# Optimization experiments

Hardware: AMD Instinct MI355X
Metric: run time of the kernel (lower is better)

The kernel has to match this reference:

```python
import jax, jax.numpy as jnp
import numpy as np

L, D, H, FF, I, MAXREL = 6, 512, 8, 2048, 50, 128
HD = D // H
NREL = 2 * MAXREL + 1
EPS = 1e-5


def setup_inputs() -> dict:
    key = jax.random.key(0)
    ks = jax.random.split(key, 32)
    s = 0.02
    p = {
        'x': jax.random.normal(ks[0], (16, 512, I), dtype=jnp.float32),
        'in_w': jax.random.normal(ks[1], (I, D)) * s,
        'in_b': jnp.zeros((D,), jnp.float32),
        'Wq': jax.random.normal(ks[2], (L, D, D)) * s,
        'Wk': jax.random.normal(ks[3], (L, D, D)) * s,
        'Wv': jax.random.normal(ks[4], (L, D, D)) * s,
        'Wo': jax.random.normal(ks[5], (L, D, D)) * s,
        'bo': jnp.zeros((L, D), jnp.float32),
        'rel_emb': jax.random.normal(ks[6], (L, NREL, HD)) * s,
        'w1': jax.random.normal(ks[7], (L, D, FF)) * s,
        'b1': jnp.zeros((L, FF), jnp.float32),
        'w2': jax.random.normal(ks[8], (L, FF, D)) * s,
        'b2': jnp.zeros((L, D), jnp.float32),
        'ln1_g': jnp.ones((L, D), jnp.float32),
        'ln1_b': jnp.zeros((L, D), jnp.float32),
        'ln2_g': jnp.ones((L, D), jnp.float32),
        'ln2_b': jnp.zeros((L, D), jnp.float32),
        'on_g': jnp.ones((D,), jnp.float32),
        'on_b': jnp.zeros((D,), jnp.float32),
        'p1_w': jax.random.normal(ks[9], (D, D // 2)) * s,
        'p1_b': jnp.zeros((D // 2,), jnp.float32),
        'p2_w': jax.random.normal(ks[10], (D // 2, 1)) * s,
        'p2_b': jnp.zeros((1,), jnp.float32),
    }
    return p


def _layer_norm(x, g, b):
    m = jnp.mean(x, axis=-1, keepdims=True)
    v = jnp.mean(jnp.square(x - m), axis=-1, keepdims=True)
    return (x - m) * jax.lax.rsqrt(v + EPS) * g + b


def _sinusoidal_pe(seq_len, d_model):
    pos = jnp.arange(seq_len, dtype=jnp.float32)[:, None]
    div = jnp.exp(jnp.arange(0, d_model, 2, dtype=jnp.float32) * (-jnp.log(10000.0) / d_model))
    pe = jnp.zeros((seq_len, d_model), jnp.float32)
    pe = pe.at[:, 0::2].set(jnp.sin(pos * div))
    pe = pe.at[:, 1::2].set(jnp.cos(pos * div))
    return pe


def reference(x, in_w, in_b, Wq, Wk, Wv, Wo, bo, rel_emb, w1, b1, w2, b2,
              ln1_g, ln1_b, ln2_g, ln2_b, on_g, on_b, p1_w, p1_b, p2_w, p2_b):
    B, S, _ = x.shape
    scale = jnp.sqrt(jnp.float32(HD))
    # relative position index matrix [S, S] in [0, 2*MAXREL]
    r = jnp.arange(S)
    rel_idx = jnp.clip(r[None, :] - r[:, None], -MAXREL, MAXREL) + MAXREL

    h = x @ in_w + in_b                       # [B,S,D]
    h = h + _sinusoidal_pe(S, D)

    for l in range(L):
        q = (h @ Wq[l]).reshape(B, S, H, HD).transpose(0, 2, 1, 3)  # [B,H,S,hd]
        k = (h @ Wk[l]).reshape(B, S, H, HD).transpose(0, 2, 1, 3)
        v = (h @ Wv[l]).reshape(B, S, H, HD).transpose(0, 2, 1, 3)
        scores = jnp.einsum('bhqd,bhkd->bhqk', q, k) / scale
        rel = rel_emb[l][rel_idx]             # [S,S,hd]
        scores = scores + jnp.einsum('bhqd,qkd->bhqk', q, rel)  # rel bias is NOT scaled (matches source)
        attn = jax.nn.softmax(scores, axis=-1)
        ctx = jnp.einsum('bhqk,bhkd->bhqd', attn, v)
        ctx = ctx.transpose(0, 2, 1, 3).reshape(B, S, D)
        attn_out = ctx @ Wo[l] + bo[l]
        h = _layer_norm(h + attn_out, ln1_g[l], ln1_b[l])
        ff = jax.nn.relu(h @ w1[l] + b1[l]) @ w2[l] + b2[l]
        h = _layer_norm(h + ff, ln2_g[l], ln2_b[l])

    h = _layer_norm(h, on_g, on_b)
    out = jax.nn.relu(h @ p1_w + p1_b) @ p2_w + p2_b  # [B,S,1]
    return out
```

## Files before the change

kernel.cpp:

```cpp
#include <hip/hip_runtime.h>

typedef unsigned short u16;
typedef unsigned int   u32;
typedef short   short8  __attribute__((ext_vector_type(8)));
typedef float   floatx4 __attribute__((ext_vector_type(4)));
typedef int     intx4   __attribute__((ext_vector_type(4)));

#define NTOK 8192
#define SEQ  512
#define NLAYER 6

#define OFF_WT   ((size_t)0)
#define OFF_HB   ((size_t)38010880)
#define OFF_QKV  ((size_t)46399488)
#define OFF_CTX  ((size_t)71565312)
#define OFF_GOUT ((size_t)79953920)
#define OFF_FF   ((size_t)96731136)
#define OFF_HD1  ((size_t)130285568)
#define OFF_VT   OFF_FF
#define OFF_RELB OFF_HD1

#define LSTRIDE 3145728
#define P1T_OFF 18874368

__device__ __forceinline__ float b2f(u16 v) { return __uint_as_float(((u32)v) << 16); }
__device__ __forceinline__ float lo16(u32 v) { return __uint_as_float(v << 16); }
__device__ __forceinline__ float hi16(u32 v) { return __uint_as_float(v & 0xffff0000u); }
__device__ __forceinline__ u16 f2b(float f) {
  u32 x = __float_as_uint(f);
  return (u16)((x + 0x7fffu + ((x >> 16) & 1u)) >> 16);
}
__device__ __forceinline__ u32 pack2(float a, float b) {
  return (u32)f2b(a) | ((u32)f2b(b) << 16);
}
__device__ __forceinline__ u32 cvtpk(float a, float b) {
  u32 r;
  asm("v_cvt_pk_bf16_f32 %0, %1, %2" : "=v"(r) : "v"(a), "v"(b));
  return r;
}

typedef __attribute__((address_space(1))) void* gas_t;
typedef __attribute__((address_space(3))) void* las_t;

__global__ __launch_bounds__(256) void transpose_all(
    const float* __restrict__ Wq, const float* __restrict__ Wk,
    const float* __restrict__ Wv, const float* __restrict__ Wo,
    const float* __restrict__ w1, const float* __restrict__ w2,
    const float* __restrict__ p1, u16* __restrict__ wT)
{
  __shared__ u16 tile[64][65];
  const int tb = blockIdx.x;
  const float* src; u16* dst; int R, C, tidx;
  if (tb < 4608) {
    const int l = tb / 768, r = tb % 768;
    const size_t lofs = (size_t)l * LSTRIDE;
    if (r < 256) {
      const int m = r >> 6; tidx = r & 63; R = 512; C = 512;
      const float* bases[4] = {Wq, Wk, Wv, Wo};
      src = bases[m] + (size_t)l * 262144;
      dst = wT + lofs + (size_t)m * 262144;
    } else if (r < 512) {
      tidx = r - 256; R = 512; C = 2048;
      src = w1 + (size_t)l * 1048576; dst = wT + lofs + 1048576;
    } else {
      tidx = r - 512; R = 2048; C = 512;
      src = w2 + (size_t)l * 1048576; dst = wT + lofs + 2097152;
    }
  } else {
    tidx = tb - 4608; R = 512; C = 256;
    src = p1; dst = wT + P1T_OFF;
  }
  const int tcn = C >> 6;
  const int tr = tidx / tcn, tc = tidx % tcn;
  const int th = threadIdx.x;
  {
    const int lr = th >> 2, cg = (th & 3) * 16;
    const float* sp = src + (size_t)(tr*64 + lr) * C + tc*64 + cg;
    float4 f0 = *(const float4*)(sp);
    float4 f1 = *(const float4*)(sp + 4);
    float4 f2 = *(const float4*)(sp + 8);
    float4 f3 = *(const float4*)(sp + 12);
    u16* tp = &tile[lr][cg];
    tp[0]=f2b(f0.x); tp[1]=f2b(f0.y); tp[2]=f2b(f0.z); tp[3]=f2b(f0.w);
    tp[4]=f2b(f1.x); tp[5]=f2b(f1.y); tp[6]=f2b(f1.z); tp[7]=f2b(f1.w);
    tp[8]=f2b(f2.x); tp[9]=f2b(f2.y); tp[10]=f2b(f2.z); tp[11]=f2b(f2.w);
    tp[12]=f2b(f3.x); tp[13]=f2b(f3.y); tp[14]=f2b(f3.z); tp[15]=f2b(f3.w);
  }
  __syncthreads();
  {
    const int oc = th >> 2, rg = (th & 3) * 16;
    u32 wds[8];
    #pragma unroll
    for (int i = 0; i < 8; ++i)
      wds[i] = (u32)tile[rg + 2*i][oc] | ((u32)tile[rg + 2*i + 1][oc] << 16);
    const int n  = tc*64 + oc;
    const int k0 = tr*64 + rg;
    const int nb = n >> 7, j = (n >> 4) & 7, lr = n & 15;
    const int kc = k0 >> 5, lq = (k0 >> 3) & 3;
    const int KC = R >> 5;
    u16* base = dst + (((((size_t)nb*KC + kc) << 3) + j) << 9);
    uint4 o0; o0.x=wds[0]; o0.y=wds[1]; o0.z=wds[2]; o0.w=wds[3];
    uint4 o1; o1.x=wds[4]; o1.y=wds[5]; o1.z=wds[6]; o1.w=wds[7];
    *(uint4*)(base + (lq*16 + lr)*8)       = o0;
    *(uint4*)(base + ((lq+1)*16 + lr)*8)   = o1;
  }
}

__global__ __launch_bounds__(128) void input_proj(
    const float* __restrict__ x, const float* __restrict__ w, const float* __restrict__ ib,
    u16* __restrict__ hb)
{
  const int row = blockIdx.x, t = threadIdx.x;
  const int s = row & (SEQ - 1);
  __shared__ float xs[50];
  if (t < 50) xs[t] = x[row*50 + t];
  __syncthreads();
  const int d0 = t * 4;
  float4 acc = *(const float4*)(ib + d0);
  #pragma unroll
  for (int i = 0; i < 50; ++i) {
    const float4 wv = *(const float4*)(w + i*512 + d0);
    const float xv = xs[i];
    acc.x = fmaf(xv, wv.x, acc.x);
    acc.y = fmaf(xv, wv.y, acc.y);
    acc.z = fmaf(xv, wv.z, acc.z);
    acc.w = fmaf(xv, wv.w, acc.w);
  }
  const float cexp = -0.017988946f;
  const float dv0 = __expf((float)d0 * cexp);
  const float dv1 = __expf((float)(d0 + 2) * cexp);
  float s0, c0, s1, c1;
  __sincosf((float)s * dv0, &s0, &c0);
  __sincosf((float)s * dv1, &s1, &c1);
  acc.x += s0; acc.y += c0; acc.z += s1; acc.w += c1;
  u32* hp = (u32*)(hb + (size_t)row*512 + d0);
  hp[0] = pack2(acc.x, acc.y);
  hp[1] = pack2(acc.z, acc.w);
}

__global__ __launch_bounds__(256, 4) void gemm_bt(
    const u16* __restrict__ A, const u16* __restrict__ Bt,
    const float* __restrict__ bias,
    u16* __restrict__ outP0, u16* __restrict__ outP1, u16* __restrict__ outB,
    u16* __restrict__ vTout,
    const int M, const int N, const int K, const int kLen, const int flags)
{
  __shared__ __align__(16) u16 As[2][8192];
  const int id = blockIdx.x;
  const int xcd = id & 7, rest = id >> 3;
  const int bm = (rest & 7) * 8 + xcd;
  const int bn = rest >> 3;
  const int z = blockIdx.y;
  const int kOff = z * kLen;
  const int m0 = bm << 7, n0 = bn << 7;
  const int tid = threadIdx.x;
  const int wave = tid >> 6, lane = tid & 63;
  const int wr = (wave >> 1) << 6, wc = (wave & 1) << 6;
  const int lrow = lane & 15, lquad = lane >> 4;

  floatx4 acc[4][4];
  #pragma unroll
  for (int i = 0; i < 4; ++i)
    #pragma unroll
    for (int j = 0; j < 4; ++j) { floatx4 zz = {0.f,0.f,0.f,0.f}; acc[i][j] = zz; }

  const u16* a0p = A + (size_t)m0 * K + kOff;
  const int c0 = tid, c1 = 256 + tid;
  const int ar0 = c0 >> 2, as0 = (c0 & 3) * 8;
  const int ar1 = c1 >> 2, as1 = (c1 & 3) * 8;
  const int KC = K >> 5;
  const u16* bW = Bt + ((((size_t)bn*KC + (kOff >> 5)) * 8 + (wave & 1) * 4) << 9) + lane*8;

#define STAGE_A(buf, k0) do {                                                                  \
    __builtin_amdgcn_global_load_lds((gas_t)(a0p + (size_t)ar0*K + (k0) + as0),                \
                                     (las_t)(&As[buf][c0*8]), 16, 0, 0);                       \
    __builtin_amdgcn_global_load_lds((gas_t)(a0p + (size_t)ar1*K + (k0) + as1),                \
                                     (las_t)(&As[buf][c1*8]), 16, 0, 0);                       \
    __builtin_amdgcn_global_load_lds((gas_t)(a0p + (size_t)ar0*K + (k0) + 32 + as0),           \
                                     (las_t)(&As[buf][4096 + c0*8]), 16, 0, 0);                \
    __builtin_amdgcn_global_load_lds((gas_t)(a0p + (size_t)ar1*K + (k0) + 32 + as1),           \
                                     (las_t)(&As[buf][4096 + c1*8]), 16, 0, 0);                \
  } while (0)

  const int nst = kLen >> 6;
  STAGE_A(0, 0);
  __syncthreads();

  int cur = 0;
  for (int t = 0; t < nst; ++t) {
    const u16* bc = bW + (size_t)(2*t) * 4096;
    short8 b0[4], b1[4];
    #pragma unroll
    for (int j = 0; j < 4; ++j) b0[j] = *(const short8*)(bc + j*512);
    if (t + 1 < nst) STAGE_A(cur ^ 1, (t + 1) * 64);
    #pragma unroll
    for (int j = 0; j < 4; ++j) b1[j] = *(const short8*)(bc + 4096 + j*512);
    {
      short8 af[4];
      #pragma unroll
      for (int i = 0; i < 4; ++i) af[i] = *(const short8*)&As[cur][(wr + i*16 + lrow)*32 + lquad*8];
      #pragma unroll
      for (int i = 0; i < 4; ++i)
        #pragma unroll
        for (int j = 0; j < 4; ++j)
          acc[i][j] = __builtin_amdgcn_mfma_f32_16x16x32_bf16(b0[j], af[i], acc[i][j], 0, 0, 0);
    }
    {
      short8 af[4];
      #pragma unroll
      for (int i = 0; i < 4; ++i) af[i] = *(const short8*)&As[cur][4096 + (wr + i*16 + lrow)*32 + lquad*8];
      #pragma unroll
      for (int i = 0; i < 4; ++i)
        #pragma unroll
        for (int j = 0; j < 4; ++j)
          acc[i][j] = __builtin_amdgcn_mfma_f32_16x16x32_bf16(b1[j], af[i], acc[i][j], 0, 0, 0);
    }
    if (t + 1 < nst) { __syncthreads(); cur ^= 1; }
  }
#undef STAGE_A

  if ((flags & 4) && n0 >= 1024) {
    #pragma unroll
    for (int i = 0; i < 4; ++i) {
      const int row = m0 + wr + i*16 + lrow;
      const int bb = row >> 9, s = row & 511;
      #pragma unroll
      for (int j = 0; j < 4; ++j) {
        const int cm0 = (n0 - 1024) + wc + j*16 + lquad*4;
        #pragma unroll
        for (int v = 0; v < 4; ++v) {
          const int cm = cm0 + v;
          const int hh = cm >> 6, d = cm & 63;
          vTout[((size_t)(bb*8 + hh)*64 + d)*512 + s] = f2b(acc[i][j][v]);
        }
      }
    }
    return;
  }

  u16* outT = outB ? outB : ((z == 0) ? outP0 : outP1);
  const bool hasb = ((flags & 1) != 0) && (z == 0);
  const bool dorelu = (flags & 2) != 0;
  #pragma unroll
  for (int i = 0; i < 4; ++i) {
    const int row = m0 + wr + i*16 + lrow;
    #pragma unroll
    for (int j = 0; j < 4; ++j) {
      const int colbase = n0 + wc + j*16 + lquad*4;
      float4 bv4 = make_float4(0.f, 0.f, 0.f, 0.f);
      if (hasb) bv4 = *(const float4*)(bias + colbase);
      float v0 = acc[i][j][0] + bv4.x;
      float v1 = acc[i][j][1] + bv4.y;
      float v2 = acc[i][j][2] + bv4.z;
      float v3 = acc[i][j][3] + bv4.w;
      if (dorelu) {
        v0 = fmaxf(v0, 0.f); v1 = fmaxf(v1, 0.f);
        v2 = fmaxf(v2, 0.f); v3 = fmaxf(v3, 0.f);
      }
      const size_t off = (size_t)row * N + colbase;
      uint2 o; o.x = pack2(v0, v1); o.y = pack2(v2, v3);
      *(uint2*)(outT + off) = o;
    }
  }
}

__global__ __launch_bounds__(256) void cvt_rel_all(
    const float* __restrict__ rel, u16* __restrict__ relB)
{
  const int i = blockIdx.x*256 + threadIdx.x;
  if (i < 6*257*64) {
    const int l = i / 16448, rem = i % 16448;
    relB[l*17408 + rem] = f2b(rel[i]);
  }
}

__global__ __launch_bounds__(256, 3) void attn_mfma(
    const u16* __restrict__ qkv, const u16* __restrict__ vT,
    const u16* __restrict__ relB, u16* __restrict__ ctx)
{
  const int id = blockIdx.x;
  const int xcd = id & 7, g = (id >> 3) & 15, qt = id >> 7;
  const int bh = xcd*16 + g;
  const int b = bh >> 3, h = bh & 7;
  const int t = threadIdx.x, w = t >> 6, lane = t & 63;
  const int lr = lane & 15, quad = lane >> 4;

  __shared__ __align__(16) u16 Ks[64*72];
  __shared__ __align__(16) u16 Vs[64*72];
  __shared__ __align__(16) u16 Pr[64*274];

  const size_t token0 = (size_t)b*512 + qt*64;
  const int srow = t >> 2, scol = (t & 3) * 16;
  const u16* kbase = qkv + (size_t)b*512*1536 + 512 + h*64;
  const u16* vbase = vT + (size_t)bh*64*512;

  short8 af0, af1;
  {
    const u16* qp = qkv + (token0 + w*16 + lr)*1536 + h*64 + quad*8;
    af0 = *(const short8*)(qp);
    af1 = *(const short8*)(qp + 32);
  }

  uint4 kr0, kr1, vr0, vr1;
  {
    const u16* kp = kbase + (size_t)srow*1536 + scol;
    kr0 = *(const uint4*)kp; kr1 = *(const uint4*)(kp + 8);
    const u16* vp = vbase + (size_t)srow*512 + scol;
    vr0 = *(const uint4*)vp; vr1 = *(const uint4*)(vp + 8);
  }

  #pragma unroll 4
  for (int nt = 0; nt < 17; ++nt) {
    const u16* rp = relB + (nt*16 + lr)*64 + quad*8;
    short8 rb0 = *(const short8*)(rp);
    short8 rb1 = *(const short8*)(rp + 32);
    floatx4 c = {0.f,0.f,0.f,0.f};
    c = __builtin_amdgcn_mfma_f32_16x16x32_bf16(af0, rb0, c, 0, 0, 0);
    c = __builtin_amdgcn_mfma_f32_16x16x32_bf16(af1, rb1, c, 0, 0, 0);
    #pragma unroll
    for (int r = 0; r < 4; ++r)
      Pr[(w*16 + quad*4 + r)*274 + nt*16 + lr] = f2b(c[r] * 1.44269504f);
  }

  floatx4 oacc[4];
  float lacc = 0.f;
  #pragma unroll
  for (int n = 0; n < 4; ++n) { floatx4 zz = {0.f,0.f,0.f,0.f}; oacc[n] = zz; }

  const int qglob = qt*64 + w*16 + lr;
  const int prbase = (w*16 + lr)*274 + 128;

  const float prLo = b2f(Pr[prbase - 128]);
  const float prHi = b2f(Pr[prbase + 128]);

  for (int kt = 0; kt < 8; ++kt) {
    __syncthreads();
    *(uint4*)&Ks[srow*72 + scol]     = kr0;
    *(uint4*)&Ks[srow*72 + scol + 8] = kr1;
    *(uint4*)&Vs[srow*72 + scol]     = vr0;
    *(uint4*)&Vs[srow*72 + scol + 8] = vr1;
    __syncthreads();

    if (kt < 7) {
      const u16* kp = kbase + (size_t)((kt+1)*64 + srow)*1536 + scol;
      kr0 = *(const uint4*)kp; kr1 = *(const uint4*)(kp + 8);
      const u16* vp = vbase + (size_t)srow*512 + (kt+1)*64 + scol;
      vr0 = *(const uint4*)vp; vr1 = *(const uint4*)(vp + 8);
    }

    floatx4 s4[4];
    __builtin_amdgcn_s_setprio(1);
    #pragma unroll
    for (int nt = 0; nt < 4; ++nt) {
      short8 kb0 = *(const short8*)&Ks[(nt*16 + lr)*72 + quad*8];
      short8 kb1 = *(const short8*)&Ks[(nt*16 + lr)*72 + 32 + quad*8];
      floatx4 c = {0.f,0.f,0.f,0.f};
      c = __builtin_amdgcn_mfma_f32_16x16x32_bf16(kb0, af0, c, 0, 0, 0);
      c = __builtin_amdgcn_mfma_f32_16x16x32_bf16(kb1, af1, c, 0, 0, 0);
      s4[nt] = c;
    }
    __builtin_amdgcn_s_setprio(0);

    const int tmin = kt*64 - (qt*64 + w*16 + 15);
    const int tmax = tmin + 78;
    u32 wq[4][2];
    const int kq = kt*64 + quad*4 - qglob;
    if (tmin >= 128 || tmax <= -128) {
      const float pc = (tmin >= 128) ? prHi : prLo;
      #pragma unroll
      for (int nt = 0; nt < 4; ++nt) {
        float p[4];
        #pragma unroll
        for (int r = 0; r < 4; ++r)
          p[r] = exp2f(fmaf(s4[nt][r], 0.18033688f, pc));
        lacc += (p[0] + p[1]) + (p[2] + p[3]);
        wq[nt][0] = cvtpk(p[0], p[1]);
        wq[nt][1] = cvtpk(p[2], p[3]);
      }
    } else if (tmin >= -128 && tmax <= 128) {
      #pragma unroll
      for (int nt = 0; nt < 4; ++nt) {
        const int dbase = kq + nt*16;
        float p[4];
        #pragma unroll
        for (int r = 0; r < 4; ++r)
          p[r] = exp2f(fmaf(s4[nt][r], 0.18033688f, b2f(Pr[prbase + dbase + r])));
        lacc += (p[0] + p[1]) + (p[2] + p[3]);
        wq[nt][0] = cvtpk(p[0], p[1]);
        wq[nt][1] = cvtpk(p[2], p[3]);
      }
    } else {
      #pragma unroll
      for (int nt = 0; nt < 4; ++nt) {
        const int dbase = kq + nt*16;
        float p[4];
        #pragma unroll
        for (int r = 0; r < 4; ++r) {
          int dd = dbase + r;
          dd = dd < -128 ? -128 : (dd > 128 ? 128 : dd);
          p[r] = exp2f(fmaf(s4[nt][r], 0.18033688f, b2f(Pr[prbase + dd])));
        }
        lacc += (p[0] + p[1]) + (p[2] + p[3]);
        wq[nt][0] = cvtpk(p[0], p[1]);
        wq[nt][1] = cvtpk(p[2], p[3]);
      }
    }

    intx4 pw0; pw0.x = (int)wq[0][0]; pw0.y = (int)wq[0][1];
               pw0.z = (int)wq[1][0]; pw0.w = (int)wq[1][1];
    intx4 pw1; pw1.x = (int)wq[2][0]; pw1.y = (int)wq[2][1];
               pw1.z = (int)wq[3][0]; pw1.w = (int)wq[3][1];
    const short8 pf0 = __builtin_bit_cast(short8, pw0);
    const short8 pf1 = __builtin_bit_cast(short8, pw1);

    __builtin_amdgcn_s_setprio(1);
    #pragma unroll
    for (int nd = 0; nd < 4; ++nd) {
      const int vrow = (nd*16 + lr)*72;
      uint2 a0 = *(const uint2*)&Vs[vrow + quad*4];
      uint2 a1 = *(const uint2*)&Vs[vrow + 16 + quad*4];
      uint2 a2 = *(const uint2*)&Vs[vrow + 32 + quad*4];
      uint2 a3 = *(const uint2*)&Vs[vrow + 48 + quad*4];
      intx4 v0; v0.x = (int)a0.x; v0.y = (int)a0.y; v0.z = (int)a1.x; v0.w = (int)a1.y;
      intx4 v1; v1.x = (int)a2.x; v1.y = (int)a2.y; v1.z = (int)a3.x; v1.w = (int)a3.y;
      const short8 vb0 = __builtin_bit_cast(short8, v0);
      const short8 vb1 = __builtin_bit_cast(short8, v1);
      oacc[nd] = __builtin_amdgcn_mfma_f32_16x16x32_bf16(vb0, pf0, oacc[nd], 0, 0, 0);
      oacc[nd] = __builtin_amdgcn_mfma_f32_16x16x32_bf16(vb1, pf1, oacc[nd], 0, 0, 0);
    }
    __builtin_amdgcn_s_setprio(0);
  }

  lacc += __shfl_xor(lacc, 16);
  lacc += __shfl_xor(lacc, 32);

  {
    const float inv = 1.f / lacc;
    u16* cp = ctx + (token0 + w*16 + lr)*512 + h*64;
    #pragma unroll
    for (int nd = 0; nd < 4; ++nd) {
      const int d = nd*16 + quad*4;
      uint2 o;
      o.x = pack2(oacc[nd][0]*inv, oacc[nd][1]*inv);
      o.y = pack2(oacc[nd][2]*inv, oacc[nd][3]*inv);
      *(uint2*)(cp + d) = o;
    }
  }
}

__global__ __launch_bounds__(256) void ln_kernel(
    const u16* __restrict__ resB, const u16* __restrict__ add0,
    const u16* __restrict__ add1,
    const float* __restrict__ g, const float* __restrict__ be,
    u16* __restrict__ hb)
{
  const int wv = threadIdx.x >> 6, ln = threadIdx.x & 63;
  const int row = blockIdx.x * 4 + wv;
  const size_t base = (size_t)row * 512;
  const int off = ln * 8;

  const uint4 rv = *(const uint4*)(resB + base + off);
  float x[8];
  x[0] = lo16(rv.x); x[1] = hi16(rv.x);
  x[2] = lo16(rv.y); x[3] = hi16(rv.y);
  x[4] = lo16(rv.z); x[5] = hi16(rv.z);
  x[6] = lo16(rv.w); x[7] = hi16(rv.w);
  if (add0) {
    const uint4 a = *(const uint4*)(add0 + base + off);
    x[0] += lo16(a.x); x[1] += hi16(a.x);
    x[2] += lo16(a.y); x[3] += hi16(a.y);
    x[4] += lo16(a.z); x[5] += hi16(a.z);
    x[6] += lo16(a.w); x[7] += hi16(a.w);
  }
  if (add1) {
    const uint4 a = *(const uint4*)(add1 + base + off);
    x[0] += lo16(a.x); x[1] += hi16(a.x);
    x[2] += lo16(a.y); x[3] += hi16(a.y);
    x[4] += lo16(a.z); x[5] += hi16(a.z);
    x[6] += lo16(a.w); x[7] += hi16(a.w);
  }

  float s = ((x[0]+x[1]) + (x[2]+x[3])) + ((x[4]+x[5]) + (x[6]+x[7]));
  #pragma unroll
  for (int o = 1; o < 64; o <<= 1) s += __shfl_xor(s, o);
  const float mean = s * (1.f/512.f);

  float vs = 0.f;
  #pragma unroll
  for (int i = 0; i < 8; ++i) { const float d = x[i] - mean; vs = fmaf(d, d, vs); }
  #pragma unroll
  for (int o = 1; o < 64; o <<= 1) vs += __shfl_xor(vs, o);
  const float inv = 1.f / sqrtf(vs * (1.f/512.f) + 1e-5f);

  const float4 g0 = *(const float4*)(g + off);
  const float4 g1 = *(const float4*)(g + off + 4);
  const float4 b0 = *(const float4*)(be + off);
  const float4 b1 = *(const float4*)(be + off + 4);
  const float y0 = (x[0]-mean)*inv*g0.x + b0.x;
  const float y1 = (x[1]-mean)*inv*g0.y + b0.y;
  const float y2 = (x[2]-mean)*inv*g0.z + b0.z;
  const float y3 = (x[3]-mean)*inv*g0.w + b0.w;
  const float y4 = (x[4]-mean)*inv*g1.x + b1.x;
  const float y5 = (x[5]-mean)*inv*g1.y + b1.y;
  const float y6 = (x[6]-mean)*inv*g1.z + b1.z;
  const float y7 = (x[7]-mean)*inv*g1.w + b1.w;
  uint4 o;
  o.x = pack2(y0, y1); o.y = pack2(y2, y3);
  o.z = pack2(y4, y5); o.w = pack2(y6, y7);
  *(uint4*)(hb + base + off) = o;
}

__global__ __launch_bounds__(256) void head2_kernel(
    const u16* __restrict__ hd1, const float* __restrict__ p2w,
    const float* __restrict__ p2b, float* __restrict__ out)
{
  const int wv = threadIdx.x >> 6, ln = threadIdx.x & 63;
  const int row = blockIdx.x * 4 + wv;
  const u16* hp = hd1 + (size_t)row * 256 + ln*4;
  const u32 h0 = *(const u32*)hp, h1 = *(const u32*)(hp + 2);
  const float4 w = *(const float4*)(p2w + ln*4);
  float acc = lo16(h0)*w.x + hi16(h0)*w.y + lo16(h1)*w.z + hi16(h1)*w.w;
  #pragma unroll
  for (int off = 1; off < 64; off <<= 1) acc += __shfl_xor(acc, off);
  if (ln == 0) out[row] = acc + p2b[0];
}

extern "C" void kernel_launch(void* const* d_in, const int* in_sizes, int n_in,
                              void* d_out, int out_size, void* d_ws, size_t ws_size,
                              hipStream_t stream) {
  (void)in_sizes; (void)n_in; (void)out_size; (void)ws_size;
  const float* X    = (const float*)d_in[0];
  const float* INW  = (const float*)d_in[1];
  const float* INB  = (const float*)d_in[2];
  const float* WQ   = (const float*)d_in[3];
  const float* WK   = (const float*)d_in[4];
  const float* WV   = (const float*)d_in[5];
  const float* WO   = (const float*)d_in[6];
  const float* BO   = (const float*)d_in[7];
  const float* REL  = (const float*)d_in[8];
  const float* W1   = (const float*)d_in[9];
  const float* B1   = (const float*)d_in[10];
  const float* W2   = (const float*)d_in[11];
  const float* B2   = (const float*)d_in[12];
  const float* LN1G = (const float*)d_in[13];
  const float* LN1B = (const float*)d_in[14];
  const float* LN2G = (const float*)d_in[15];
  const float* LN2B = (const float*)d_in[16];
  const float* ONG  = (const float*)d_in[17];
  const float* ONB  = (const float*)d_in[18];
  const float* P1W  = (const float*)d_in[19];
  const float* P1B  = (const float*)d_in[20];
  const float* P2W  = (const float*)d_in[21];
  const float* P2B  = (const float*)d_in[22];
  float* out = (float*)d_out;

  char* ws = (char*)d_ws;
  u16*   wT    = (u16*)(ws + OFF_WT);
  u16*   hB    = (u16*)(ws + OFF_HB);
  u16*   qkv   = (u16*)(ws + OFF_QKV);
  u16*   ctx   = (u16*)(ws + OFF_CTX);
  u16*   gout0 = (u16*)(ws + OFF_GOUT);
  u16*   gout1 = (u16*)(ws + OFF_QKV);
  u16*   ff    = (u16*)(ws + OFF_FF);
  u16*   hd1   = (u16*)(ws + OFF_HD1);
  u16*   vTb   = (u16*)(ws + OFF_VT);
  u16*   relBa = (u16*)(ws + OFF_RELB);

  transpose_all<<<4640, 256, 0, stream>>>(WQ, WK, WV, WO, W1, W2, P1W, wT);
  cvt_rel_all<<<386, 256, 0, stream>>>(REL, relBa);
  input_proj<<<NTOK, 128, 0, stream>>>(X, INW, INB, hB);

  for (int l = 0; l < NLAYER; ++l) {
    const u16* wTl = wT + (size_t)l * LSTRIDE;
    gemm_bt<<<dim3(768,1), 256, 0, stream>>>(hB, wTl, nullptr, nullptr, nullptr, qkv, vTb,
                                             8192, 1536, 512, 512, 4);
    attn_mfma<<<1024, 256, 0, stream>>>(qkv, vTb, relBa + l*17408, ctx);
    gemm_bt<<<dim3(256,2), 256, 0, stream>>>(ctx, wTl + 786432, BO + l*512,
                                             gout0, gout1, nullptr, nullptr,
                                             8192, 512, 512, 256, 1);
    ln_kernel<<<2048, 256, 0, stream>>>(hB, gout0, gout1, LN1G + l*512, LN1B + l*512, hB);
    gemm_bt<<<dim3(1024,1), 256, 0, stream>>>(hB, wTl + 1048576, B1 + l*2048,
                                              nullptr, nullptr, ff, nullptr,
                                              8192, 2048, 512, 512, 3);
    gemm_bt<<<dim3(256,2), 256, 0, stream>>>(ff, wTl + 2097152, B2 + l*512,
                                             gout0, gout1, nullptr, nullptr,
                                             8192, 512, 2048, 1024, 1);
    ln_kernel<<<2048, 256, 0, stream>>>(hB, gout0, gout1, LN2G + l*512, LN2B + l*512, hB);
  }
  ln_kernel<<<2048, 256, 0, stream>>>(hB, nullptr, nullptr, ONG, ONB, hB);
  gemm_bt<<<dim3(128,1), 256, 0, stream>>>(hB, wT + P1T_OFF, P1B,
                                           nullptr, nullptr, hd1, nullptr,
                                           8192, 256, 512, 512, 3);
  head2_kernel<<<2048, 256, 0, stream>>>(hd1, P2W, P2B, out);
}
```

Baseline: 1.075 ms.

## Store activations in MFMA-packed layout and load GEMM A operand directly

Activations (hidden state, attention context, FF intermediate) are now written by producer kernels in the same fragment-packed layout already used for the transposed weights. This lets the GEMM load A fragments straight from global memory into registers, like B, and drop the LDS staging buffer and its barriers. The GEMM main loop is rewritten as a register double buffer, and the occupancy hint drops from 4 to 3 blocks to make room for the extra registers. The cost is scattered packed-index stores in the producers and more global traffic per wave, since nothing is shared through LDS.

```diff
diff --git a/kernel.cpp b/kernel.cpp
--- a/kernel.cpp
+++ b/kernel.cpp
@@ -11,10 +11,10 @@
 #define NLAYER 6
 
 #define OFF_WT   ((size_t)0)
-#define OFF_HB   ((size_t)38010880)
 #define OFF_QKV  ((size_t)46399488)
 #define OFF_CTX  ((size_t)71565312)
 #define OFF_GOUT ((size_t)79953920)
+#define OFF_HBP  ((size_t)88342528)
 #define OFF_FF   ((size_t)96731136)
 #define OFF_HD1  ((size_t)130285568)
 #define OFF_VT   OFF_FF
@@ -37,6 +37,10 @@
   u32 r;
   asm("v_cvt_pk_bf16_f32 %0, %1, %2" : "=v"(r) : "v"(a), "v"(b));
   return r;
+}
+__device__ __forceinline__ size_t packIdx(int m, int k, int KC) {
+  return ((((size_t)(m >> 7) * KC + (k >> 5)) * 8 + ((m >> 4) & 7)) << 9)
+         + (size_t)((((k >> 3) & 3) * 16 + (m & 15)) * 8 + (k & 7));
 }
 
 typedef __attribute__((address_space(1))) void* gas_t;
@@ -108,7 +112,7 @@
 
 __global__ __launch_bounds__(128) void input_proj(
     const float* __restrict__ x, const float* __restrict__ w, const float* __restrict__ ib,
-    u16* __restrict__ hb)
+    u16* __restrict__ hbp)
 {
   const int row = blockIdx.x, t = threadIdx.x;
   const int s = row & (SEQ - 1);
@@ -133,19 +137,18 @@
   __sincosf((float)s * dv0, &s0, &c0);
   __sincosf((float)s * dv1, &s1, &c1);
   acc.x += s0; acc.y += c0; acc.z += s1; acc.w += c1;
-  u32* hp = (u32*)(hb + (size_t)row*512 + d0);
-  hp[0] = pack2(acc.x, acc.y);
-  hp[1] = pack2(acc.z, acc.w);
-}
-
-__global__ __launch_bounds__(256, 4) void gemm_bt(
+  uint2 o; o.x = pack2(acc.x, acc.y); o.y = pack2(acc.z, acc.w);
+  *(uint2*)(hbp + packIdx(row, d0, 16)) = o;
+}
+
+__global__ __launch_bounds__(256, 3) void gemm_bt(
     const u16* __restrict__ A, const u16* __restrict__ Bt,
     const float* __restrict__ bias,
     u16* __restrict__ outP0, u16* __restrict__ outP1, u16* __restrict__ outB,
     u16* __restrict__ vTout,
     const int M, const int N, const int K, const int kLen, const int flags)
 {
-  __shared__ __align__(16) u16 As[2][8192];
+  (void)M;
   const int id = blockIdx.x;
   const int xcd = id & 7, rest = id >> 3;
   const int bm = (rest & 7) * 8 + xcd;
@@ -164,60 +167,43 @@
     #pragma unroll
     for (int j = 0; j < 4; ++j) { floatx4 zz = {0.f,0.f,0.f,0.f}; acc[i][j] = zz; }
 
-  const u16* a0p = A + (size_t)m0 * K + kOff;
-  const int c0 = tid, c1 = 256 + tid;
-  const int ar0 = c0 >> 2, as0 = (c0 & 3) * 8;
-  const int ar1 = c1 >> 2, as1 = (c1 & 3) * 8;
   const int KC = K >> 5;
+  const u16* aW = A  + ((((size_t)bm*KC + (kOff >> 5)) * 8 + (wave >> 1) * 4) << 9) + lane*8;
   const u16* bW = Bt + ((((size_t)bn*KC + (kOff >> 5)) * 8 + (wave & 1) * 4) << 9) + lane*8;
 
-#define STAGE_A(buf, k0) do {                                                                  \
-    __builtin_amdgcn_global_load_lds((gas_t)(a0p + (size_t)ar0*K + (k0) + as0),                \
-                                     (las_t)(&As[buf][c0*8]), 16, 0, 0);                       \
-    __builtin_amdgcn_global_load_lds((gas_t)(a0p + (size_t)ar1*K + (k0) + as1),                \
-                                     (las_t)(&As[buf][c1*8]), 16, 0, 0);                       \
-    __builtin_amdgcn_global_load_lds((gas_t)(a0p + (size_t)ar0*K + (k0) + 32 + as0),           \
-                                     (las_t)(&As[buf][4096 + c0*8]), 16, 0, 0);                \
-    __builtin_amdgcn_global_load_lds((gas_t)(a0p + (size_t)ar1*K + (k0) + 32 + as1),           \
-                                     (las_t)(&As[buf][4096 + c1*8]), 16, 0, 0);                \
-  } while (0)
-
   const int nst = kLen >> 6;
-  STAGE_A(0, 0);
-  __syncthreads();
-
-  int cur = 0;
+  short8 aA[4], bA[4], aB[4], bB[4];
+  #pragma unroll
+  for (int i = 0; i < 4; ++i) {
+    aA[i] = *(const short8*)(aW + i*512);
+    bA[i] = *(const short8*)(bW + i*512);
+  }
   for (int t = 0; t < nst; ++t) {
-    const u16* bc = bW + (size_t)(2*t) * 4096;
-    short8 b0[4], b1[4];
-    #pragma unroll
-    for (int j = 0; j < 4; ++j) b0[j] = *(const short8*)(bc + j*512);
-    if (t + 1 < nst) STAGE_A(cur ^ 1, (t + 1) * 64);
-    #pragma unroll
-    for (int j = 0; j < 4; ++j) b1[j] = *(const short8*)(bc + 4096 + j*512);
-    {
-      short8 af[4];
-      #pragma unroll
-      for (int i = 0; i < 4; ++i) af[i] = *(const short8*)&As[cur][(wr + i*16 + lrow)*32 + lquad*8];
-      #pragma unroll
-      for (int i = 0; i < 4; ++i)
-        #pragma unroll
-        for (int j = 0; j < 4; ++j)
-          acc[i][j] = __builtin_amdgcn_mfma_f32_16x16x32_bf16(b0[j], af[i], acc[i][j], 0, 0, 0);
-    }
-    {
-      short8 af[4];
-      #pragma unroll
-      for (int i = 0; i < 4; ++i) af[i] = *(const short8*)&As[cur][4096 + (wr + i*16 + lrow)*32 + lquad*8];
-      #pragma unroll
-      for (int i = 0; i < 4; ++i)
-        #pragma unroll
-        for (int j = 0; j < 4; ++j)
-          acc[i][j] = __builtin_amdgcn_mfma_f32_16x16x32_bf16(b1[j], af[i], acc[i][j], 0, 0, 0);
-    }
-    if (t + 1 < nst) { __syncthreads(); cur ^= 1; }
-  }
-#undef STAGE_A
+    const size_t o1 = (size_t)(2*t + 1) * 4096;
+    #pragma unroll
+    for (int i = 0; i < 4; ++i) {
+      aB[i] = *(const short8*)(aW + o1 + i*512);
+      bB[i] = *(const short8*)(bW + o1 + i*512);
+    }
+    #pragma unroll
+    for (int i = 0; i < 4; ++i)
+      #pragma unroll
+      for (int j = 0; j < 4; ++j)
+        acc[i][j] = __builtin_amdgcn_mfma_f32_16x16x32_bf16(bA[j], aA[i], acc[i][j], 0, 0, 0);
+    if (t + 1 < nst) {
+      const size_t o2 = (size_t)(2*t + 2) * 4096;
+      #pragma unroll
+      for (int i = 0; i < 4; ++i) {
+        aA[i] = *(const short8*)(aW + o2 + i*512);
+        bA[i] = *(const short8*)(bW + o2 + i*512);
+      }
+    }
+    #pragma unroll
+    for (int i = 0; i < 4; ++i)
+      #pragma unroll
+      for (int j = 0; j < 4; ++j)
+        acc[i][j] = __builtin_amdgcn_mfma_f32_16x16x32_bf16(bB[j], aB[i], acc[i][j], 0, 0, 0);
+  }
 
   if ((flags & 4) && n0 >= 1024) {
     #pragma unroll
@@ -241,6 +227,8 @@
   u16* outT = outB ? outB : ((z == 0) ? outP0 : outP1);
   const bool hasb = ((flags & 1) != 0) && (z == 0);
   const bool dorelu = (flags & 2) != 0;
+  const bool opack = (flags & 8) != 0;
+  const int KCo = N >> 5;
   #pragma unroll
   for (int i = 0; i < 4; ++i) {
     const int row = m0 + wr + i*16 + lrow;
@@ -257,7 +245,8 @@
         v0 = fmaxf(v0, 0.f); v1 = fmaxf(v1, 0.f);
         v2 = fmaxf(v2, 0.f); v3 = fmaxf(v3, 0.f);
       }
-      const size_t off = (size_t)row * N + colbase;
+      const size_t off = opack ? packIdx(row, colbase, KCo)
+                               : (size_t)row * N + colbase;
       uint2 o; o.x = pack2(v0, v1); o.y = pack2(v2, v3);
       *(uint2*)(outT + off) = o;
     }
@@ -436,30 +425,31 @@
 
   {
     const float inv = 1.f / lacc;
-    u16* cp = ctx + (token0 + w*16 + lr)*512 + h*64;
+    const int tok = (int)token0 + w*16 + lr;
     #pragma unroll
     for (int nd = 0; nd < 4; ++nd) {
-      const int d = nd*16 + quad*4;
+      const int k = h*64 + nd*16 + quad*4;
       uint2 o;
       o.x = pack2(oacc[nd][0]*inv, oacc[nd][1]*inv);
       o.y = pack2(oacc[nd][2]*inv, oacc[nd][3]*inv);
-      *(uint2*)(cp + d) = o;
+      *(uint2*)(ctx + packIdx(tok, k, 16)) = o;
     }
   }
 }
 
 __global__ __launch_bounds__(256) void ln_kernel(
-    const u16* __restrict__ resB, const u16* __restrict__ add0,
+    const u16* __restrict__ resP, const u16* __restrict__ add0,
     const u16* __restrict__ add1,
     const float* __restrict__ g, const float* __restrict__ be,
-    u16* __restrict__ hb)
+    u16* __restrict__ hbp)
 {
   const int wv = threadIdx.x >> 6, ln = threadIdx.x & 63;
   const int row = blockIdx.x * 4 + wv;
   const size_t base = (size_t)row * 512;
   const int off = ln * 8;
-
-  const uint4 rv = *(const uint4*)(resB + base + off);
+  const size_t pidx = packIdx(row, off, 16);
+
+  const uint4 rv = *(const uint4*)(resP + pidx);
   float x[8];
   x[0] = lo16(rv.x); x[1] = hi16(rv.x);
   x[2] = lo16(rv.y); x[3] = hi16(rv.y);
@@ -507,7 +497,7 @@
   uint4 o;
   o.x = pack2(y0, y1); o.y = pack2(y2, y3);
   o.z = pack2(y4, y5); o.w = pack2(y6, y7);
-  *(uint4*)(hb + base + off) = o;
+  *(uint4*)(hbp + pidx) = o;
 }
 
 __global__ __launch_bounds__(256) void head2_kernel(
@@ -556,11 +546,11 @@
 
   char* ws = (char*)d_ws;
   u16*   wT    = (u16*)(ws + OFF_WT);
-  u16*   hB    = (u16*)(ws + OFF_HB);
   u16*   qkv   = (u16*)(ws + OFF_QKV);
   u16*   ctx   = (u16*)(ws + OFF_CTX);
   u16*   gout0 = (u16*)(ws + OFF_GOUT);
   u16*   gout1 = (u16*)(ws + OFF_QKV);
+  u16*   hBp   = (u16*)(ws + OFF_HBP);
   u16*   ff    = (u16*)(ws + OFF_FF);
   u16*   hd1   = (u16*)(ws + OFF_HD1);
   u16*   vTb   = (u16*)(ws + OFF_VT);
@@ -568,27 +558,27 @@
 
   transpose_all<<<4640, 256, 0, stream>>>(WQ, WK, WV, WO, W1, W2, P1W, wT);
   cvt_rel_all<<<386, 256, 0, stream>>>(REL, relBa);
-  input_proj<<<NTOK, 128, 0, stream>>>(X, INW, INB, hB);
+  input_proj<<<NTOK, 128, 0, stream>>>(X, INW, INB, hBp);
 
   for (int l = 0; l < NLAYER; ++l) {
     const u16* wTl = wT + (size_t)l * LSTRIDE;
-    gemm_bt<<<dim3(768,1), 256, 0, stream>>>(hB, wTl, nullptr, nullptr, nullptr, qkv, vTb,
+    gemm_bt<<<dim3(768,1), 256, 0, stream>>>(hBp, wTl, nullptr, nullptr, nullptr, qkv, vTb,
                                              8192, 1536, 512, 512, 4);
     attn_mfma<<<1024, 256, 0, stream>>>(qkv, vTb, relBa + l*17408, ctx);
     gemm_bt<<<dim3(256,2), 256, 0, stream>>>(ctx, wTl + 786432, BO + l*512,
                                              gout0, gout1, nullptr, nullptr,
                                              8192, 512, 512, 256, 1);
-    ln_kernel<<<2048, 256, 0, stream>>>(hB, gout0, gout1, LN1G + l*512, LN1B + l*512, hB);
-    gemm_bt<<<dim3(1024,1), 256, 0, stream>>>(hB, wTl + 1048576, B1 + l*2048,
+    ln_kernel<<<2048, 256, 0, stream>>>(hBp, gout0, gout1, LN1G + l*512, LN1B + l*512, hBp);
+    gemm_bt<<<dim3(1024,1), 256, 0, stream>>>(hBp, wTl + 1048576, B1 + l*2048,
                                               nullptr, nullptr, ff, nullptr,
-                                              8192, 2048, 512, 512, 3);
+                                              8192, 2048, 512, 512, 11);
     gemm_bt<<<dim3(256,2), 256, 0, stream>>>(ff, wTl + 2097152, B2 + l*512,
                                              gout0, gout1, nullptr, nullptr,
                                              8192, 512, 2048, 1024, 1);
-    ln_kernel<<<2048, 256, 0, stream>>>(hB, gout0, gout1, LN2G + l*512, LN2B + l*512, hB);
-  }
-  ln_kernel<<<2048, 256, 0, stream>>>(hB, nullptr, nullptr, ONG, ONB, hB);
-  gemm_bt<<<dim3(128,1), 256, 0, stream>>>(hB, wT + P1T_OFF, P1B,
+    ln_kernel<<<2048, 256, 0, stream>>>(hBp, gout0, gout1, LN2G + l*512, LN2B + l*512, hBp);
+  }
+  ln_kernel<<<2048, 256, 0, stream>>>(hBp, nullptr, nullptr, ONG, ONB, hBp);
+  gemm_bt<<<dim3(128,1), 256, 0, stream>>>(hBp, wT + P1T_OFF, P1B,
                                            nullptr, nullptr, hd1, nullptr,
                                            8192, 256, 512, 512, 3);
   head2_kernel<<<2048, 256, 0, stream>>>(hd1, P2W, P2B, out);
```

New measurement: 1.205 ms. +12.1%, slower.
